# Kernel tuning notes

Hardware: AMD Instinct MI355X
Metric: run time of the kernel (lower is better)

## Reference

```python
import jax, jax.numpy as jnp
import numpy as np

B, N, C_IN, T = 16, 1024, 16, 36
K, C_OUT = 3, 64


def setup_inputs() -> dict:
    key = jax.random.key(0)
    k1, k2, k3, k4 = jax.random.split(key, 4)
    x = jax.random.normal(k1, (B, N, C_IN, T), dtype=jnp.float32)
    spatial_attention = jax.random.uniform(k2, (B, N, N), dtype=jnp.float32)
    cheb = jax.random.normal(k3, (K, N, N), dtype=jnp.float32) * 0.1
    theta = jax.random.normal(k4, (K, C_IN, C_OUT), dtype=jnp.float32) * 0.1
    return {"x": x, "spatial_attention": spatial_attention, "cheb": cheb, "theta": theta}


def reference(x, spatial_attention, cheb, theta):
    # x: [B,N,C_in,T], spatial_attention: [B,N,N], cheb: [K,N,N], theta: [K,C_in,C_out]
    # Original: per (t,k): ((T_k * SAt).T @ x[..., t]) @ theta_k, summed over k, ReLU.
    # Compute attention-weighted adjacency ONCE (time-invariant), batch over all t.
    t_at = cheb[:, None, :, :] * spatial_attention[None]          # [K,B,N,N]
    # rhs[k,b,n,c,t] = sum_m t_at[k,b,m,n] * x[b,m,c,t]  (permute(0,2,1).matmul)
    rhs = jnp.einsum('kbmn,bmct->kbnct', t_at, x)                 # [K,B,N,C_in,T]
    out = jnp.einsum('kbnct,kco->bnot', rhs, theta)               # [B,N,C_out,T]
    return jax.nn.relu(out)
```

## Files before the change

### kernel.cpp

```cpp
#include <hip/hip_runtime.h>
#include <hip/hip_bf16.h>

#define NB 16
#define NN 1024
#define CIN 16
#define TT 36
#define KK 3
#define COUT 64
#define CT 576
#define KB 48

typedef __attribute__((ext_vector_type(8))) short bf16x8;
typedef __attribute__((ext_vector_type(4))) float f32x4;

__device__ __forceinline__ unsigned short f2bf(float f) {
    union { float f; unsigned int u; } v; v.f = f;
    unsigned int r = v.u + 0x7FFF + ((v.u >> 16) & 1);
    return (unsigned short)(r >> 16);
}

__global__ __launch_bounds__(256) void prep_a(const float* __restrict__ cheb,
                                              const float* __restrict__ sat,
                                              ushort* __restrict__ At,
                                              int n_base, int rows) {
    __shared__ ushort tile[64][68];
    const int ntiles = rows >> 6;
    const int k = blockIdx.y;
    const int n0 = n_base + (blockIdx.x % ntiles) * 64;
    const int m0 = (blockIdx.x / ntiles) * 64;
    const int tid = threadIdx.x;

    size_t goff[4];
    float4 cv[4], sv[4];
#pragma unroll
    for (int i = 0; i < 4; ++i) {
        int f = i * 256 + tid;
        goff[i] = (size_t)(m0 + (f >> 4)) * NN + n0 + ((f & 15) << 2);
        cv[i] = *(const float4*)(cheb + (size_t)k * NN * NN + goff[i]);
        sv[i] = *(const float4*)(sat + goff[i]);
    }
    for (int b = 0; b < 16; ++b) {
#pragma unroll
        for (int i = 0; i < 4; ++i) {
            int f = i * 256 + tid;
            ushort4 u;
            u.x = f2bf(cv[i].x * sv[i].x); u.y = f2bf(cv[i].y * sv[i].y);
            u.z = f2bf(cv[i].z * sv[i].z); u.w = f2bf(cv[i].w * sv[i].w);
            *(ushort4*)&tile[f >> 4][(f & 15) << 2] = u;
        }
        if (b < 15) {
            const float* sa = sat + (size_t)(b + 1) * NN * NN;
#pragma unroll
            for (int i = 0; i < 4; ++i) sv[i] = *(const float4*)(sa + goff[i]);
        }
        __syncthreads();
        ushort* outp = At + (size_t)(k * 16 + b) * rows * NN;
#pragma unroll
        for (int i = 0; i < 4; ++i) {
            int f = i * 256 + tid;
            int n = f >> 4, m4 = (f & 15) << 2;
            ushort4 u;
            u.x = tile[m4 + 0][n]; u.y = tile[m4 + 1][n];
            u.z = tile[m4 + 2][n]; u.w = tile[m4 + 3][n];
            *(ushort4*)(outp + (size_t)(n0 - n_base + n) * NN + m0 + m4) = u;
        }
        __syncthreads();
    }
}

__global__ __launch_bounds__(256) void prep_x(const float* __restrict__ x,
                                              ushort* __restrict__ Xt) {
    __shared__ ushort tile[64][68];
    const int b = blockIdx.y;
    const int m0 = (blockIdx.x & 15) * 64;
    const int c0 = (blockIdx.x >> 4) * 64;
    const int tid = threadIdx.x;
    const float* xb = x + (size_t)b * NN * CT;
#pragma unroll
    for (int i = 0; i < 4; ++i) {
        int f = i * 256 + tid;
        int mr = f >> 4, c4 = (f & 15) << 2;
        float4 v = *(const float4*)(xb + (size_t)(m0 + mr) * CT + c0 + c4);
        ushort4 u;
        u.x = f2bf(v.x); u.y = f2bf(v.y); u.z = f2bf(v.z); u.w = f2bf(v.w);
        *(ushort4*)&tile[mr][c4] = u;
    }
    __syncthreads();
    ushort* outp = Xt + (size_t)b * CT * NN;
#pragma unroll
    for (int i = 0; i < 4; ++i) {
        int f = i * 256 + tid;
        int n = f >> 4, m4 = (f & 15) << 2;
        int ctlin = c0 + n;
        int c = ctlin / 36, t = ctlin - 36 * c;
        int ctp = t * 16 + c;
        ushort4 u;
        u.x = tile[m4 + 0][n]; u.y = tile[m4 + 1][n];
        u.z = tile[m4 + 2][n]; u.w = tile[m4 + 3][n];
        *(ushort4*)(outp + (size_t)ctp * NN + m0 + m4) = u;
    }
}

__global__ __launch_bounds__(512) void gemm1(const ushort* __restrict__ At,
                                             const ushort* __restrict__ Xt,
                                             ushort* __restrict__ rhs2,
                                             int nsplit, int n_base, int rows) {
    __shared__ ushort lds[2 * 320 * 64];
    const int tid = threadIdx.x;
    const int y = blockIdx.y;
    const int b = y / 3, k = y - 3 * b;
    const int l = k * 16 + b;
    const int ntiles = rows >> 7;
    const int nt = blockIdx.x % ntiles;
    const int ctt = blockIdx.x / ntiles;
    const int nloc0 = nt * 128;
    const int ct0 = ctt * 192;
    const ushort* Ab = At + ((size_t)l * (nsplit ? rows : NN) + nloc0) * NN;
    const ushort* Bb = Xt + (size_t)b * CT * NN + (size_t)ct0 * NN;

    const int srow = tid >> 3;
    const int schunk = tid & 7;
    const int swz = schunk ^ (srow & 7);
    const ushort* a_src0 = Ab + (size_t)srow * NN + swz * 8;
    const ushort* b_src0 = Bb + (size_t)srow * NN + swz * 8;

    auto STAGE = [&](int kt, int p) {
        const int mk = kt * 64;
        ushort* base = lds + p * (320 * 64);
        const ushort* as = a_src0 + mk;
        const ushort* bs = b_src0 + mk;
#pragma unroll
        for (int i = 0; i < 2; ++i)
            __builtin_amdgcn_global_load_lds(
                (const __attribute__((address_space(1))) void*)(as + (size_t)i * 64 * NN),
                (__attribute__((address_space(3))) void*)(base + (tid + i * 512) * 8), 16, 0, 0);
#pragma unroll
        for (int i = 0; i < 3; ++i)
            __builtin_amdgcn_global_load_lds(
                (const __attribute__((address_space(1))) void*)(bs + (size_t)i * 64 * NN),
                (__attribute__((address_space(3))) void*)(base + 128 * 64 + (tid + i * 512) * 8), 16, 0, 0);
    };

    const int w = tid >> 6, lane = tid & 63;
    const int wr = w >> 2, wc = w & 3;
    const int lrow = lane & 15, quad = lane >> 4;
    const int koff0 = ((quad ^ (lrow & 7)) << 3);
    f32x4 acc[4][3] = {};

    STAGE(0, 0);
    STAGE(1, 1);
    asm volatile("s_waitcnt vmcnt(5)\n\ts_barrier" ::: "memory");

    for (int kt = 0; kt < 16; ++kt) {
        const int p = kt & 1;
        const ushort* bufA = lds + p * (320 * 64);
        const ushort* bufB = bufA + 128 * 64;
#pragma unroll
        for (int kp = 0; kp < 2; ++kp) {
            const int koff = koff0 ^ (kp << 5);
            bf16x8 af[4], bfr[3];
#pragma unroll
            for (int mi = 0; mi < 4; ++mi)
                af[mi] = *(const bf16x8*)&bufA[(wr * 64 + mi * 16 + lrow) * 64 + koff];
#pragma unroll
            for (int ni = 0; ni < 3; ++ni)
                bfr[ni] = *(const bf16x8*)&bufB[(wc * 48 + ni * 16 + lrow) * 64 + koff];
            __builtin_amdgcn_s_setprio(1);
#pragma unroll
            for (int mi = 0; mi < 4; ++mi)
#pragma unroll
                for (int ni = 0; ni < 3; ++ni)
                    acc[mi][ni] = __builtin_amdgcn_mfma_f32_16x16x32_bf16(
                        af[mi], bfr[ni], acc[mi][ni], 0, 0, 0);
            __builtin_amdgcn_s_setprio(0);
        }
        asm volatile("s_barrier" ::: "memory");
        if (kt + 2 < 16) {
            STAGE(kt + 2, p);
            asm volatile("s_waitcnt vmcnt(5)\n\ts_barrier" ::: "memory");
        } else if (kt + 1 < 16) {
            asm volatile("s_waitcnt vmcnt(0)\n\ts_barrier" ::: "memory");
        }
    }

    ushort* cs = lds;
#pragma unroll
    for (int mi = 0; mi < 4; ++mi)
#pragma unroll
        for (int ni = 0; ni < 3; ++ni)
#pragma unroll
            for (int r = 0; r < 4; ++r)
                cs[(wr * 64 + mi * 16 + quad * 4 + r) * 200 + wc * 48 + ni * 16 + lrow] =
                    f2bf(acc[mi][ni][r]);
    __syncthreads();

    for (int f = tid; f < 1536; f += 512) {
        int n = f / 12, tl = f - 12 * (f / 12);
        int t = ctt * 12 + tl;
        uint4 v0 = *(const uint4*)&cs[n * 200 + tl * 16];
        uint4 v1 = *(const uint4*)&cs[n * 200 + tl * 16 + 8];
        size_t g = (((size_t)b * NN + n_base + nloc0 + n) * 36 + t) * 48 + k * 16;
        *(uint4*)(rhs2 + g) = v0;
        *(uint4*)(rhs2 + g + 8) = v1;
    }
}

__global__ __launch_bounds__(256) void apply_mfma2(const ushort* __restrict__ rhs2,
                                                   const float* __restrict__ theta,
                                                   float* __restrict__ out) {
    __shared__ ushort thT[64 * 72];
    __shared__ float ostage[4][64 * 36];
    const int tid = threadIdx.x;
    for (int f = tid; f < 64 * 64; f += 256) {
        int o = f >> 6, kc = f & 63;
        thT[o * 72 + kc] = f2bf((kc < 48) ? theta[kc * 64 + o] : 0.f);
    }
    __syncthreads();
    const int w = tid >> 6, lane = tid & 63;
    const int lrow = lane & 15, quad = lane >> 4;

    bf16x8 a[4][2];
#pragma unroll
    for (int mi = 0; mi < 4; ++mi)
#pragma unroll
        for (int kc = 0; kc < 2; ++kc)
            a[mi][kc] = *(const bf16x8*)&thT[(mi * 16 + lrow) * 72 + kc * 32 + quad * 8];

    float* ost = &ostage[w][0];
    for (int j = 0; j < 4; ++j) {
        const int bn = blockIdx.x * 16 + w * 4 + j;
        const ushort* rrow = rhs2 + (size_t)bn * (36 * 48);
        f32x4 acc[4][3] = {};
#pragma unroll
        for (int ni = 0; ni < 3; ++ni)
#pragma unroll
            for (int kc = 0; kc < 2; ++kc) {
                bf16x8 bf = *(const bf16x8*)(rrow + (ni * 16 + lrow) * 48 + kc * 32 + quad * 8);
#pragma unroll
                for (int mi = 0; mi < 4; ++mi)
                    acc[mi][ni] = __builtin_amdgcn_mfma_f32_16x16x32_bf16(
                        a[mi][kc], bf, acc[mi][ni], 0, 0, 0);
            }
#pragma unroll
        for (int mi = 0; mi < 4; ++mi)
#pragma unroll
            for (int ni = 0; ni < 3; ++ni)
#pragma unroll
                for (int r = 0; r < 4; ++r) {
                    int t = ni * 16 + lrow;
                    if (t < 36)
                        ost[(mi * 16 + quad * 4 + r) * 36 + t] = fmaxf(acc[mi][ni][r], 0.f);
                }
        asm volatile("s_waitcnt lgkmcnt(0)" ::: "memory");
        float* ob = out + (size_t)bn * (COUT * TT);
#pragma unroll
        for (int q = 0; q < 9; ++q) {
            int f = q * 64 + lane;
            *(float4*)&ob[f * 4] = *(const float4*)&ost[f * 4];
        }
    }
}

__global__ __launch_bounds__(256) void naive_fused(const float* __restrict__ x,
                                                   const float* __restrict__ sat,
                                                   const float* __restrict__ cheb,
                                                   const float* __restrict__ theta,
                                                   float* __restrict__ out) {
    __shared__ float wgt[3][1024];
    __shared__ float rs[3][576];
    const int tid = threadIdx.x;
    const int n = blockIdx.x, b = blockIdx.y;
    for (int f = tid; f < 3 * 1024; f += 256) {
        int k = f >> 10, m = f & 1023;
        wgt[k][m] = cheb[(size_t)k * NN * NN + (size_t)m * NN + n] *
                    sat[(size_t)b * NN * NN + (size_t)m * NN + n];
    }
    __syncthreads();
    float a0[3] = {}, a1[3] = {}, a2[3] = {};
    const float* xb = x + (size_t)b * NN * CT;
    for (int m = 0; m < 1024; ++m) {
        const float* xr = xb + (size_t)m * CT;
        float x0 = xr[tid];
        float x1 = xr[256 + tid];
        float x2 = (tid < 64) ? xr[512 + tid] : 0.f;
#pragma unroll
        for (int k = 0; k < 3; ++k) {
            float wm = wgt[k][m];
            a0[k] += wm * x0; a1[k] += wm * x1; a2[k] += wm * x2;
        }
    }
#pragma unroll
    for (int k = 0; k < 3; ++k) {
        rs[k][tid] = a0[k];
        rs[k][256 + tid] = a1[k];
        if (tid < 64) rs[k][512 + tid] = a2[k];
    }
    __syncthreads();
    const int o = tid >> 2, tg = tid & 3;
    float oa[9] = {};
    for (int kc = 0; kc < 48; ++kc) {
        int k = kc >> 4, c = kc & 15;
        float th = theta[kc * 64 + o];
        const float* rp = &rs[k][c * TT + tg * 9];
#pragma unroll
        for (int j = 0; j < 9; ++j) oa[j] += th * rp[j];
    }
    float* ob = out + ((size_t)b * NN + n) * (COUT * TT);
#pragma unroll
    for (int j = 0; j < 9; ++j)
        ob[o * TT + tg * 9 + j] = fmaxf(oa[j], 0.f);
}

extern "C" void kernel_launch(void* const* d_in, const int* in_sizes, int n_in,
                              void* d_out, int out_size, void* d_ws, size_t ws_size,
                              hipStream_t stream) {
    const float* x     = (const float*)d_in[0];
    const float* sat   = (const float*)d_in[1];
    const float* cheb  = (const float*)d_in[2];
    const float* theta = (const float*)d_in[3];
    float* out = (float*)d_out;

    const size_t RHS2 = (size_t)NB * NN * 36 * 48;
    const size_t XT   = (size_t)NB * CT * NN;
    const size_t ATF  = (size_t)KB * NN * NN;
    const size_t ATNS = (size_t)KB * 512 * NN;
    const size_t needA     = (RHS2 + XT + ATF) * 2;
    const size_t needSplit = (RHS2 + XT + ATNS) * 2;

    ushort* rhs2 = (ushort*)d_ws;
    ushort* Xt   = rhs2 + RHS2;
    ushort* At   = Xt + XT;

    if (ws_size >= needA) {
        prep_x<<<dim3(144, NB), 256, 0, stream>>>(x, Xt);
        prep_a<<<dim3(256, KK), 256, 0, stream>>>(cheb, sat, At, 0, 1024);
        gemm1<<<dim3(24, KB), 512, 0, stream>>>(At, Xt, rhs2, 0, 0, 1024);
        apply_mfma2<<<dim3(NB * NN / 16), 256, 0, stream>>>(rhs2, theta, out);
    } else if (ws_size >= needSplit) {
        prep_x<<<dim3(144, NB), 256, 0, stream>>>(x, Xt);
        for (int half = 0; half < 2; ++half) {
            int nb = half * 512;
            prep_a<<<dim3(128, KK), 256, 0, stream>>>(cheb, sat, At, nb, 512);
            gemm1<<<dim3(12, KB), 512, 0, stream>>>(At, Xt, rhs2, 1, nb, 512);
        }
        apply_mfma2<<<dim3(NB * NN / 16), 256, 0, stream>>>(rhs2, theta, out);
    } else {
        naive_fused<<<dim3(NN, NB), 256, 0, stream>>>(x, sat, cheb, theta, out);
    }
}
```

Baseline: 384.9 us.

## Fuse theta projection into graph GEMM, computing all three Chebyshev orders per block

```diff
diff --git a/kernel.cpp b/kernel.cpp
--- a/kernel.cpp
+++ b/kernel.cpp
@@ -101,164 +101,144 @@
     }
 }
 
-__global__ __launch_bounds__(512) void gemm1(const ushort* __restrict__ At,
-                                             const ushort* __restrict__ Xt,
-                                             ushort* __restrict__ rhs2,
-                                             int nsplit, int n_base, int rows) {
-    __shared__ ushort lds[2 * 320 * 64];
+__global__ __launch_bounds__(512) void gemm1f(const ushort* __restrict__ At,
+                                              const ushort* __restrict__ Xt,
+                                              const float* __restrict__ theta,
+                                              float* __restrict__ out,
+                                              int nsplit, int n_base, int rows) {
+    __shared__ ushort lds[2 * 384 * 64];
+    __shared__ ushort thT[64 * 72];
     const int tid = threadIdx.x;
-    const int y = blockIdx.y;
-    const int b = y / 3, k = y - 3 * b;
-    const int l = k * 16 + b;
-    const int ntiles = rows >> 7;
+    const int b = blockIdx.y;
+    const int ntiles = rows >> 6;
     const int nt = blockIdx.x % ntiles;
     const int ctt = blockIdx.x / ntiles;
-    const int nloc0 = nt * 128;
+    const int nloc0 = nt * 64;
     const int ct0 = ctt * 192;
-    const ushort* Ab = At + ((size_t)l * (nsplit ? rows : NN) + nloc0) * NN;
-    const ushort* Bb = Xt + (size_t)b * CT * NN + (size_t)ct0 * NN;
-
-    const int srow = tid >> 3;
-    const int schunk = tid & 7;
+    const int atrows = nsplit ? rows : NN;
+
+    for (int f = tid; f < 64 * 64; f += 512) {
+        int o = f >> 6, kc = f & 63;
+        thT[o * 72 + kc] = f2bf((kc < 48) ? theta[kc * 64 + o] : 0.f);
+    }
+
+    const int srow = tid >> 3, schunk = tid & 7;
     const int swz = schunk ^ (srow & 7);
-    const ushort* a_src0 = Ab + (size_t)srow * NN + swz * 8;
-    const ushort* b_src0 = Bb + (size_t)srow * NN + swz * 8;
+    const ushort* a_src[3];
+#pragma unroll
+    for (int k = 0; k < 3; ++k)
+        a_src[k] = At + ((size_t)(k * 16 + b) * atrows + nloc0 + srow) * NN + swz * 8;
+    const ushort* b_src = Xt + (size_t)b * CT * NN + (size_t)(ct0 + srow) * NN + swz * 8;
 
     auto STAGE = [&](int kt, int p) {
         const int mk = kt * 64;
-        ushort* base = lds + p * (320 * 64);
-        const ushort* as = a_src0 + mk;
-        const ushort* bs = b_src0 + mk;
-#pragma unroll
-        for (int i = 0; i < 2; ++i)
+        ushort* base = lds + p * (384 * 64);
+#pragma unroll
+        for (int k = 0; k < 3; ++k)
             __builtin_amdgcn_global_load_lds(
-                (const __attribute__((address_space(1))) void*)(as + (size_t)i * 64 * NN),
-                (__attribute__((address_space(3))) void*)(base + (tid + i * 512) * 8), 16, 0, 0);
+                (const __attribute__((address_space(1))) void*)(a_src[k] + mk),
+                (__attribute__((address_space(3))) void*)(base + k * 4096 + tid * 8), 16, 0, 0);
 #pragma unroll
         for (int i = 0; i < 3; ++i)
             __builtin_amdgcn_global_load_lds(
-                (const __attribute__((address_space(1))) void*)(bs + (size_t)i * 64 * NN),
-                (__attribute__((address_space(3))) void*)(base + 128 * 64 + (tid + i * 512) * 8), 16, 0, 0);
+                (const __attribute__((address_space(1))) void*)(b_src + (size_t)i * 64 * NN + mk),
+                (__attribute__((address_space(3))) void*)(base + 3 * 4096 + (tid + i * 512) * 8), 16, 0, 0);
     };
 
     const int w = tid >> 6, lane = tid & 63;
     const int wr = w >> 2, wc = w & 3;
     const int lrow = lane & 15, quad = lane >> 4;
-    const int koff0 = ((quad ^ (lrow & 7)) << 3);
-    f32x4 acc[4][3] = {};
+    const int s3 = lrow & 7;
+    f32x4 acc[3][2][3] = {};
 
     STAGE(0, 0);
     STAGE(1, 1);
-    asm volatile("s_waitcnt vmcnt(5)\n\ts_barrier" ::: "memory");
+    asm volatile("s_waitcnt vmcnt(6)\n\ts_barrier" ::: "memory");
 
     for (int kt = 0; kt < 16; ++kt) {
         const int p = kt & 1;
-        const ushort* bufA = lds + p * (320 * 64);
-        const ushort* bufB = bufA + 128 * 64;
+        const ushort* bufA = lds + p * (384 * 64);
+        const ushort* bufB = bufA + 3 * 4096;
 #pragma unroll
         for (int kp = 0; kp < 2; ++kp) {
-            const int koff = koff0 ^ (kp << 5);
-            bf16x8 af[4], bfr[3];
-#pragma unroll
-            for (int mi = 0; mi < 4; ++mi)
-                af[mi] = *(const bf16x8*)&bufA[(wr * 64 + mi * 16 + lrow) * 64 + koff];
+            const int koff = (((kp * 4 + quad) ^ s3) << 3);
+            bf16x8 af[3][2], bfr[3];
+#pragma unroll
+            for (int k = 0; k < 3; ++k)
+#pragma unroll
+                for (int mi = 0; mi < 2; ++mi)
+                    af[k][mi] = *(const bf16x8*)&bufA[k * 4096 + (wr * 32 + mi * 16 + lrow) * 64 + koff];
 #pragma unroll
             for (int ni = 0; ni < 3; ++ni)
                 bfr[ni] = *(const bf16x8*)&bufB[(wc * 48 + ni * 16 + lrow) * 64 + koff];
             __builtin_amdgcn_s_setprio(1);
 #pragma unroll
-            for (int mi = 0; mi < 4; ++mi)
-#pragma unroll
-                for (int ni = 0; ni < 3; ++ni)
-                    acc[mi][ni] = __builtin_amdgcn_mfma_f32_16x16x32_bf16(
-                        af[mi], bfr[ni], acc[mi][ni], 0, 0, 0);
+            for (int k = 0; k < 3; ++k)
+#pragma unroll
+                for (int mi = 0; mi < 2; ++mi)
+#pragma unroll
+                    for (int ni = 0; ni < 3; ++ni)
+                        acc[k][mi][ni] = __builtin_amdgcn_mfma_f32_16x16x32_bf16(
+                            af[k][mi], bfr[ni], acc[k][mi][ni], 0, 0, 0);
             __builtin_amdgcn_s_setprio(0);
         }
         asm volatile("s_barrier" ::: "memory");
         if (kt + 2 < 16) {
             STAGE(kt + 2, p);
-            asm volatile("s_waitcnt vmcnt(5)\n\ts_barrier" ::: "memory");
+            asm volatile("s_waitcnt vmcnt(6)\n\ts_barrier" ::: "memory");
         } else if (kt + 1 < 16) {
             asm volatile("s_waitcnt vmcnt(0)\n\ts_barrier" ::: "memory");
         }
     }
 
-    ushort* cs = lds;
-#pragma unroll
-    for (int mi = 0; mi < 4; ++mi)
-#pragma unroll
-        for (int ni = 0; ni < 3; ++ni)
-#pragma unroll
-            for (int r = 0; r < 4; ++r)
-                cs[(wr * 64 + mi * 16 + quad * 4 + r) * 200 + wc * 48 + ni * 16 + lrow] =
-                    f2bf(acc[mi][ni][r]);
-    __syncthreads();
-
-    for (int f = tid; f < 1536; f += 512) {
-        int n = f / 12, tl = f - 12 * (f / 12);
-        int t = ctt * 12 + tl;
-        uint4 v0 = *(const uint4*)&cs[n * 200 + tl * 16];
-        uint4 v1 = *(const uint4*)&cs[n * 200 + tl * 16 + 8];
-        size_t g = (((size_t)b * NN + n_base + nloc0 + n) * 36 + t) * 48 + k * 16;
-        *(uint4*)(rhs2 + g) = v0;
-        *(uint4*)(rhs2 + g + 8) = v1;
-    }
-}
-
-__global__ __launch_bounds__(256) void apply_mfma2(const ushort* __restrict__ rhs2,
-                                                   const float* __restrict__ theta,
-                                                   float* __restrict__ out) {
-    __shared__ ushort thT[64 * 72];
-    __shared__ float ostage[4][64 * 36];
-    const int tid = threadIdx.x;
-    for (int f = tid; f < 64 * 64; f += 256) {
-        int o = f >> 6, kc = f & 63;
-        thT[o * 72 + kc] = f2bf((kc < 48) ? theta[kc * 64 + o] : 0.f);
-    }
-    __syncthreads();
-    const int w = tid >> 6, lane = tid & 63;
-    const int lrow = lane & 15, quad = lane >> 4;
-
-    bf16x8 a[4][2];
-#pragma unroll
-    for (int mi = 0; mi < 4; ++mi)
-#pragma unroll
-        for (int kc = 0; kc < 2; ++kc)
-            a[mi][kc] = *(const bf16x8*)&thT[(mi * 16 + lrow) * 72 + kc * 32 + quad * 8];
-
-    float* ost = &ostage[w][0];
-    for (int j = 0; j < 4; ++j) {
-        const int bn = blockIdx.x * 16 + w * 4 + j;
-        const ushort* rrow = rhs2 + (size_t)bn * (36 * 48);
-        f32x4 acc[4][3] = {};
-#pragma unroll
-        for (int ni = 0; ni < 3; ++ni)
-#pragma unroll
-            for (int kc = 0; kc < 2; ++kc) {
-                bf16x8 bf = *(const bf16x8*)(rrow + (ni * 16 + lrow) * 48 + kc * 32 + quad * 8);
-#pragma unroll
-                for (int mi = 0; mi < 4; ++mi)
-                    acc[mi][ni] = __builtin_amdgcn_mfma_f32_16x16x32_bf16(
-                        a[mi][kc], bf, acc[mi][ni], 0, 0, 0);
+    ushort* rst = lds + w * 6144;
+#pragma unroll
+    for (int k = 0; k < 3; ++k) {
+        const int chunk = k * 2 + (lrow >> 3);
+#pragma unroll
+        for (int mi = 0; mi < 2; ++mi)
+#pragma unroll
+            for (int ni = 0; ni < 3; ++ni)
+#pragma unroll
+                for (int r = 0; r < 4; ++r) {
+                    int nrow = mi * 16 + quad * 4 + r;
+                    rst[ni * 2048 + nrow * 64 + ((chunk ^ (nrow & 7)) << 3) + s3] =
+                        f2bf(acc[k][mi][ni][r]);
+                }
+    }
+    bf16x8 a_th[4][2];
+#pragma unroll
+    for (int of = 0; of < 4; ++of)
+#pragma unroll
+        for (int ks = 0; ks < 2; ++ks)
+            a_th[of][ks] = *(const bf16x8*)&thT[(of * 16 + lrow) * 72 + ks * 32 + quad * 8];
+
+    const int n_g0 = n_base + nloc0 + wr * 32 + lrow;
+    const int t_g0 = ctt * 12 + wc * 3;
+    float* ob = out + (size_t)b * NN * (COUT * TT);
+#pragma unroll
+    for (int ni = 0; ni < 3; ++ni)
+#pragma unroll
+        for (int nf = 0; nf < 2; ++nf) {
+            f32x4 o4[4] = {};
+#pragma unroll
+            for (int ks = 0; ks < 2; ++ks) {
+                bf16x8 bfr = *(const bf16x8*)&rst[ni * 2048 + (nf * 16 + lrow) * 64 +
+                                                 (((ks * 4 + quad) ^ s3) << 3)];
+#pragma unroll
+                for (int of = 0; of < 4; ++of)
+                    o4[of] = __builtin_amdgcn_mfma_f32_16x16x32_bf16(
+                        a_th[of][ks], bfr, o4[of], 0, 0, 0);
             }
-#pragma unroll
-        for (int mi = 0; mi < 4; ++mi)
-#pragma unroll
-            for (int ni = 0; ni < 3; ++ni)
+            size_t nb2 = (size_t)(n_g0 + nf * 16) * (COUT * TT);
+#pragma unroll
+            for (int of = 0; of < 4; ++of)
 #pragma unroll
                 for (int r = 0; r < 4; ++r) {
-                    int t = ni * 16 + lrow;
-                    if (t < 36)
-                        ost[(mi * 16 + quad * 4 + r) * 36 + t] = fmaxf(acc[mi][ni][r], 0.f);
+                    int o = of * 16 + quad * 4 + r;
+                    ob[nb2 + (size_t)o * TT + t_g0 + ni] = fmaxf(o4[of][r], 0.f);
                 }
-        asm volatile("s_waitcnt lgkmcnt(0)" ::: "memory");
-        float* ob = out + (size_t)bn * (COUT * TT);
-#pragma unroll
-        for (int q = 0; q < 9; ++q) {
-            int f = q * 64 + lane;
-            *(float4*)&ob[f * 4] = *(const float4*)&ost[f * 4];
-        }
-    }
+        }
 }
 
 __global__ __launch_bounds__(256) void naive_fused(const float* __restrict__ x,
@@ -320,30 +300,26 @@
     const float* theta = (const float*)d_in[3];
     float* out = (float*)d_out;
 
-    const size_t RHS2 = (size_t)NB * NN * 36 * 48;
     const size_t XT   = (size_t)NB * CT * NN;
     const size_t ATF  = (size_t)KB * NN * NN;
     const size_t ATNS = (size_t)KB * 512 * NN;
-    const size_t needA     = (RHS2 + XT + ATF) * 2;
-    const size_t needSplit = (RHS2 + XT + ATNS) * 2;
-
-    ushort* rhs2 = (ushort*)d_ws;
-    ushort* Xt   = rhs2 + RHS2;
-    ushort* At   = Xt + XT;
+    const size_t needA     = (XT + ATF) * 2;
+    const size_t needSplit = (XT + ATNS) * 2;
+
+    ushort* Xt = (ushort*)d_ws;
+    ushort* At = Xt + XT;
 
     if (ws_size >= needA) {
         prep_x<<<dim3(144, NB), 256, 0, stream>>>(x, Xt);
         prep_a<<<dim3(256, KK), 256, 0, stream>>>(cheb, sat, At, 0, 1024);
-        gemm1<<<dim3(24, KB), 512, 0, stream>>>(At, Xt, rhs2, 0, 0, 1024);
-        apply_mfma2<<<dim3(NB * NN / 16), 256, 0, stream>>>(rhs2, theta, out);
+        gemm1f<<<dim3(48, NB), 512, 0, stream>>>(At, Xt, theta, out, 0, 0, 1024);
     } else if (ws_size >= needSplit) {
         prep_x<<<dim3(144, NB), 256, 0, stream>>>(x, Xt);
         for (int half = 0; half < 2; ++half) {
             int nb = half * 512;
             prep_a<<<dim3(128, KK), 256, 0, stream>>>(cheb, sat, At, nb, 512);
-            gemm1<<<dim3(12, KB), 512, 0, stream>>>(At, Xt, rhs2, 1, nb, 512);
-        }
-        apply_mfma2<<<dim3(NB * NN / 16), 256, 0, stream>>>(rhs2, theta, out);
+            gemm1f<<<dim3(24, NB), 512, 0, stream>>>(At, Xt, theta, out, 1, nb, 512);
+        }
     } else {
         naive_fused<<<dim3(NN, NB), 256, 0, stream>>>(x, sat, cheb, theta, out);
     }
```

New measurement: 494.4 us. 28.5% more time.
